# Kernel optimization log

Hardware: AMD Instinct MI355X
Metric: run time of the kernel (lower is better)

The kernel has to match this reference:

```python
import jax, jax.numpy as jnp
import numpy as np

HEADS = 16
EMBD = 1024
D_K = EMBD // HEADS


def setup_inputs() -> dict:
    key = jax.random.key(0)
    ks = jax.random.split(key, 9)
    s = 1.0 / np.sqrt(EMBD)
    inp = {
        "x": jax.random.normal(ks[0], (4, 2048, EMBD), dtype=jnp.float32),
        "w_q": jax.random.normal(ks[1], (EMBD, EMBD), dtype=jnp.float32) * s,
        "b_q": jax.random.normal(ks[2], (EMBD,), dtype=jnp.float32) * 0.01,
        "w_k": jax.random.normal(ks[3], (EMBD, EMBD), dtype=jnp.float32) * s,
        "b_k": jax.random.normal(ks[4], (EMBD,), dtype=jnp.float32) * 0.01,
        "w_v": jax.random.normal(ks[5], (EMBD, EMBD), dtype=jnp.float32) * s,
        "b_v": jax.random.normal(ks[6], (EMBD,), dtype=jnp.float32) * 0.01,
        "w_o": jax.random.normal(ks[7], (EMBD, EMBD), dtype=jnp.float32) * s,
        "b_o": jax.random.normal(ks[8], (EMBD,), dtype=jnp.float32) * 0.01,
    }
    return inp


def reference(x, w_q, b_q, w_k, b_k, w_v, b_v, w_o, b_o):
    b, s, e = x.shape
    # Linear layers (torch Linear: x @ W^T + b; weights stored as [out,in] -> here [in,out] already? We store [in,out])
    q = x @ w_q + b_q
    k = x @ w_k + b_k
    v = x @ w_v + b_v
    # reshape to [b, h, s, d_k]
    qh = q.reshape(b, s, HEADS, D_K).transpose(0, 2, 1, 3)
    kh = k.reshape(b, s, HEADS, D_K).transpose(0, 2, 1, 3)
    vh = v.reshape(b, s, HEADS, D_K).transpose(0, 2, 1, 3)
    scores = jnp.einsum('bhqd,bhkd->bhqk', qh, kh) / jnp.sqrt(jnp.asarray(D_K, x.dtype))
    attn = jax.nn.softmax(scores, axis=-1)
    out = jnp.einsum('bhqk,bhkd->bhqd', attn, vh)
    merged = out.transpose(0, 2, 1, 3).reshape(b, s, e)
    return merged @ w_o + b_o
```

## Files before the change

kernel.cpp:

```cpp
#include <hip/hip_runtime.h>
#include <math.h>

#define B 4
#define S 2048
#define E 1024
#define H 16
#define DK 64
#define NROW (B * S)
#define NT (S / 64)

typedef _Float16 half_t;
typedef __attribute__((ext_vector_type(8))) _Float16 half8;
typedef __attribute__((ext_vector_type(4))) _Float16 half4;
typedef __attribute__((ext_vector_type(4))) float f32x4;

__device__ __forceinline__ void gload_lds16(const void* g, void* l) {
    __builtin_amdgcn_global_load_lds((__attribute__((address_space(1))) void*)(g),
                                     (__attribute__((address_space(3))) void*)(l), 16, 0, 0);
}

__device__ __forceinline__ float fast_exp2(float x) {
    return __builtin_amdgcn_exp2f(x);
}

__global__ __launch_bounds__(256)
void cast_x_kernel(const float* __restrict__ x, half_t* __restrict__ xh) {
    const size_t i = ((size_t)blockIdx.x * 256 + threadIdx.x) * 8;
    float4 a = *(const float4*)(x + i);
    float4 b = *(const float4*)(x + i + 4);
    half8 hv;
    hv[0] = (half_t)a.x; hv[1] = (half_t)a.y; hv[2] = (half_t)a.z; hv[3] = (half_t)a.w;
    hv[4] = (half_t)b.x; hv[5] = (half_t)b.y; hv[6] = (half_t)b.z; hv[7] = (half_t)b.w;
    *(half8*)(xh + i) = hv;
}

__global__ __launch_bounds__(256)
void cast_wT_kernel(const float* __restrict__ w0, const float* __restrict__ w1,
                    const float* __restrict__ w2, const float* __restrict__ w3,
                    half_t* __restrict__ o0, half_t* __restrict__ o1,
                    half_t* __restrict__ o2, half_t* __restrict__ o3) {
    __shared__ half_t Ts[64][72];
    const int z = blockIdx.z;
    const float* W = (z == 0) ? w0 : (z == 1) ? w1 : (z == 2) ? w2 : w3;
    half_t*      O = (z == 0) ? o0 : (z == 1) ? o1 : (z == 2) ? o2 : o3;
    const int t  = threadIdx.x;
    const int k0 = blockIdx.y * 64;
    const int n0 = blockIdx.x * 64;
    const int r  = t >> 2;
    const int c0 = (t & 3) * 16;
    const float* p = W + (size_t)(k0 + r) * E + n0 + c0;
    #pragma unroll
    for (int j = 0; j < 16; j += 4) {
        float4 v = *(const float4*)(p + j);
        Ts[c0 + j + 0][r] = (half_t)v.x;
        Ts[c0 + j + 1][r] = (half_t)v.y;
        Ts[c0 + j + 2][r] = (half_t)v.z;
        Ts[c0 + j + 3][r] = (half_t)v.w;
    }
    __syncthreads();
    half_t* q = O + (size_t)(n0 + r) * E + k0 + c0;
    *(uint4*)(q)     = *(const uint4*)&Ts[r][c0];
    *(uint4*)(q + 8) = *(const uint4*)&Ts[r][c0 + 8];
}

__global__ __launch_bounds__(256)
void gemm_qkv_kernel(const half_t* __restrict__ A, const half_t* __restrict__ Bt,
                     const float* __restrict__ b_q, const float* __restrict__ b_k,
                     const float* __restrict__ b_v,
                     half_t* __restrict__ Qh, half_t* __restrict__ Kh,
                     half_t* __restrict__ Vt) {
    __shared__ half_t SM[128 * 136];
    const int t    = threadIdx.x;
    const int w    = t >> 6;
    const int lane = t & 63;
    const int ln   = t & 15;
    const int qd   = (t >> 4) & 3;
    const int orig = blockIdx.y * 24 + blockIdx.x;
    const int swz  = (orig & 7) * 192 + (orig >> 3);
    const int bn0  = (swz % 24) * 128;
    const int bm0  = (swz / 24) * 128;
    const int wm   = (w & 1) * 64;
    const int wn   = (w >> 1) * 64;
    const int srow = lane >> 2;
    const int sch  = (((lane & 3) ^ (srow & 3)) * 8);
    const int rch  = ((qd ^ (ln & 3)) * 8);

    f32x4 acc[4][4];
    #pragma unroll
    for (int mi = 0; mi < 4; ++mi)
        #pragma unroll
        for (int ni = 0; ni < 4; ++ni) acc[mi][ni] = (f32x4){0.f, 0.f, 0.f, 0.f};

    for (int k0 = 0; k0 < E; k0 += 64) {
        #pragma unroll
        for (int kh = 0; kh < 2; ++kh)
            #pragma unroll
            for (int c = 0; c < 2; ++c) {
                const int rr = c * 64 + w * 16;
                gload_lds16(A  + (size_t)(bm0 + rr + srow) * E + k0 + kh * 32 + sch,
                            SM + kh * 4096 + rr * 32);
                gload_lds16(Bt + (size_t)(bn0 + rr + srow) * E + k0 + kh * 32 + sch,
                            SM + 8192 + kh * 4096 + rr * 32);
            }
        __syncthreads();
        #pragma unroll
        for (int kh = 0; kh < 2; ++kh) {
            half8 af[4], bf[4];
            #pragma unroll
            for (int mi = 0; mi < 4; ++mi)
                af[mi] = *(const half8*)&SM[kh * 4096 + (wm + mi * 16 + ln) * 32 + rch];
            #pragma unroll
            for (int ni = 0; ni < 4; ++ni)
                bf[ni] = *(const half8*)&SM[8192 + kh * 4096 + (wn + ni * 16 + ln) * 32 + rch];
            #pragma unroll
            for (int mi = 0; mi < 4; ++mi)
                #pragma unroll
                for (int ni = 0; ni < 4; ++ni)
                    acc[mi][ni] = __builtin_amdgcn_mfma_f32_16x16x32_f16(af[mi], bf[ni], acc[mi][ni], 0, 0, 0);
        }
        __syncthreads();
    }

    const int route = bn0 >> 10;
    const int nloc0 = bn0 & 1023;
    const float* bp = (route == 0) ? b_q : (route == 1) ? b_k : b_v;
    float bv[4];
    #pragma unroll
    for (int ni = 0; ni < 4; ++ni) bv[ni] = bp[nloc0 + wn + ni * 16 + ln];

    if (route < 2) {
        half_t* Cst = (route == 0) ? Qh : Kh;
        #pragma unroll
        for (int mi = 0; mi < 4; ++mi)
            #pragma unroll
            for (int r = 0; r < 4; ++r) {
                const size_t row = (size_t)(bm0 + wm + mi * 16 + qd * 4 + r);
                #pragma unroll
                for (int ni = 0; ni < 4; ++ni)
                    Cst[row * E + nloc0 + wn + ni * 16 + ln] = (half_t)(acc[mi][ni][r] + bv[ni]);
            }
    } else {
        #pragma unroll
        for (int mi = 0; mi < 4; ++mi)
            #pragma unroll
            for (int ni = 0; ni < 4; ++ni)
                #pragma unroll
                for (int r = 0; r < 4; ++r)
                    SM[(wn + ni * 16 + ln) * 136 + wm + mi * 16 + qd * 4 + r] =
                        (half_t)(acc[mi][ni][r] + bv[ni]);
        __syncthreads();
        const int nl = t >> 1;
        const int sc = (t & 1) * 64;
        const int gv = nloc0 + nl;
        const int hh = gv >> 6, dd = gv & 63;
        const int bb = bm0 >> 11;
        const int sb = (bm0 & (S - 1)) + sc;
        half_t* dst = Vt + ((size_t)(bb * H + hh) * DK + dd) * S + sb;
        const half_t* src = SM + nl * 136 + sc;
        #pragma unroll
        for (int j = 0; j < 64; j += 8)
            *(half8*)(dst + j) = *(const half8*)(src + j);
    }
}

__global__ __launch_bounds__(256)
void gemm_oproj_kernel(const half_t* __restrict__ A, const half_t* __restrict__ Bt,
                       const float* __restrict__ bias, float* __restrict__ Cout) {
    __shared__ half_t SM[2 * 8192];
    const int t    = threadIdx.x;
    const int w    = t >> 6;
    const int lane = t & 63;
    const int ln   = t & 15;
    const int qd   = (t >> 4) & 3;
    const int orig = blockIdx.y * 8 + blockIdx.x;
    const int swz  = (orig & 7) * 64 + (orig >> 3);
    const int bn0  = (swz & 7) * 128;
    const int bm0  = (swz >> 3) * 128;
    const int wm   = (w & 1) * 64;
    const int wn   = (w >> 1) * 64;
    const int srow = lane >> 2;
    const int sch  = (((lane & 3) ^ (srow & 3)) * 8);
    const int rch  = ((qd ^ (ln & 3)) * 8);

    f32x4 acc[4][4];
    #pragma unroll
    for (int mi = 0; mi < 4; ++mi)
        #pragma unroll
        for (int ni = 0; ni < 4; ++ni) acc[mi][ni] = (f32x4){0.f, 0.f, 0.f, 0.f};

    for (int k0 = 0; k0 < E; k0 += 64) {
        #pragma unroll
        for (int kh = 0; kh < 2; ++kh)
            #pragma unroll
            for (int c = 0; c < 2; ++c) {
                const int rr = c * 64 + w * 16;
                gload_lds16(A  + (size_t)(bm0 + rr + srow) * E + k0 + kh * 32 + sch,
                            SM + kh * 4096 + rr * 32);
                gload_lds16(Bt + (size_t)(bn0 + rr + srow) * E + k0 + kh * 32 + sch,
                            SM + 8192 + kh * 4096 + rr * 32);
            }
        __syncthreads();
        #pragma unroll
        for (int kh = 0; kh < 2; ++kh) {
            half8 af[4], bf[4];
            #pragma unroll
            for (int mi = 0; mi < 4; ++mi)
                af[mi] = *(const half8*)&SM[kh * 4096 + (wm + mi * 16 + ln) * 32 + rch];
            #pragma unroll
            for (int ni = 0; ni < 4; ++ni)
                bf[ni] = *(const half8*)&SM[8192 + kh * 4096 + (wn + ni * 16 + ln) * 32 + rch];
            #pragma unroll
            for (int mi = 0; mi < 4; ++mi)
                #pragma unroll
                for (int ni = 0; ni < 4; ++ni)
                    acc[mi][ni] = __builtin_amdgcn_mfma_f32_16x16x32_f16(af[mi], bf[ni], acc[mi][ni], 0, 0, 0);
        }
        __syncthreads();
    }

    float bv[4];
    #pragma unroll
    for (int ni = 0; ni < 4; ++ni) bv[ni] = bias[bn0 + wn + ni * 16 + ln];
    #pragma unroll
    for (int mi = 0; mi < 4; ++mi)
        #pragma unroll
        for (int r = 0; r < 4; ++r) {
            const size_t row = (size_t)(bm0 + wm + mi * 16 + qd * 4 + r);
            #pragma unroll
            for (int ni = 0; ni < 4; ++ni)
                Cout[row * E + bn0 + wn + ni * 16 + ln] = acc[mi][ni][r] + bv[ni];
        }
}

__global__ __launch_bounds__(256, 4)
void attn_kernel7(const half_t* __restrict__ Qg, const half_t* __restrict__ Kg,
                  const half_t* __restrict__ Vtg, half_t* __restrict__ CTX) {
    __shared__ half_t Kbuf[2][4096];
    __shared__ half_t Vbuf[2][4096];

    const int t    = threadIdx.x;
    const int w    = t >> 6;
    const int lane = t & 63;
    const int ln   = t & 15;
    const int qd   = (t >> 4) & 3;
    const int orig = blockIdx.y * 16 + blockIdx.x;
    const int swz  = (orig & 7) * 128 + (orig >> 3);
    const int bh   = swz >> 4;
    const int s0   = (swz & 15) * 128;
    const int b    = bh >> 4;
    const int h    = bh & 15;
    const int q0   = w * 32;

    half8 aq[2][2];
    #pragma unroll
    for (int mt = 0; mt < 2; ++mt)
        #pragma unroll
        for (int kd = 0; kd < 2; ++kd)
            aq[mt][kd] = *(const half8*)(Qg +
                (size_t)(b * S + s0 + q0 + mt * 16 + ln) * E + h * DK + kd * 32 + qd * 8);

    const half_t* kgp = Kg + (size_t)(b * S + w * 16 + ln) * E + h * DK + qd * 8;
    const half_t* vgp = Vtg + (size_t)(bh * DK + w * 16 + (lane & 7)) * S + (lane >> 3) * 8;

    gload_lds16(kgp,      &Kbuf[0][(w * 2 + 0) * 512]);
    gload_lds16(kgp + 32, &Kbuf[0][(w * 2 + 1) * 512]);
    gload_lds16(vgp,                 &Vbuf[0][(w * 2 + 0) * 512]);
    gload_lds16(vgp + (size_t)8 * S, &Vbuf[0][(w * 2 + 1) * 512]);

    f32x4 oacc[2][4];
    #pragma unroll
    for (int mt = 0; mt < 2; ++mt)
        #pragma unroll
        for (int dt = 0; dt < 4; ++dt) oacc[mt][dt] = (f32x4){0.f, 0.f, 0.f, 0.f};
    f32x4 lfrag[2];
    lfrag[0] = (f32x4){0.f, 0.f, 0.f, 0.f};
    lfrag[1] = (f32x4){0.f, 0.f, 0.f, 0.f};

    half8 vone;
    #pragma unroll
    for (int j = 0; j < 8; ++j) vone[j] = (half_t)1;

    const float kexp  = 0.1803368731f;
    const float kbias = 7.2134752f;

    const int vrb = (ln >> 3) * 512 + (ln & 7) * 8 + (qd & 1) * 4 + (qd >> 1) * 64;

    for (int kt = 0; kt < NT; ++kt) {
        const int cur = kt & 1;
        __syncthreads();

        if (kt + 1 < NT) {
            const half_t* kp = kgp + (size_t)(kt + 1) * 64 * E;
            const half_t* vp = vgp + (kt + 1) * 64;
            gload_lds16(kp,      &Kbuf[1 - cur][(w * 2 + 0) * 512]);
            gload_lds16(kp + 32, &Kbuf[1 - cur][(w * 2 + 1) * 512]);
            gload_lds16(vp,                 &Vbuf[1 - cur][(w * 2 + 0) * 512]);
            gload_lds16(vp + (size_t)8 * S, &Vbuf[1 - cur][(w * 2 + 1) * 512]);
        }

        half8 kf[4][2];
        #pragma unroll
        for (int ct = 0; ct < 4; ++ct)
            #pragma unroll
            for (int kd = 0; kd < 2; ++kd)
                kf[ct][kd] = *(const half8*)&Kbuf[cur][(ct * 2 + kd) * 512 + lane * 8];

        half8 vf[4][2];
        const half_t* vb = &Vbuf[cur][vrb];
        #pragma unroll
        for (int dt = 0; dt < 4; ++dt)
            #pragma unroll
            for (int kq = 0; kq < 2; ++kq) {
                union { half4 h4[2]; half8 h8; } u;
                u.h4[0] = *(const half4*)(vb + dt * 1024 + kq * 256);
                u.h4[1] = *(const half4*)(vb + dt * 1024 + kq * 256 + 128);
                vf[dt][kq] = u.h8;
            }

        #pragma unroll
        for (int mt = 0; mt < 2; ++mt) {
            f32x4 sacc[4];
            #pragma unroll
            for (int ct = 0; ct < 4; ++ct) {
                f32x4 sv = (f32x4){0.f, 0.f, 0.f, 0.f};
                sv = __builtin_amdgcn_mfma_f32_16x16x32_f16(kf[ct][0], aq[mt][0], sv, 0, 0, 0);
                sv = __builtin_amdgcn_mfma_f32_16x16x32_f16(kf[ct][1], aq[mt][1], sv, 0, 0, 0);
                sacc[ct] = sv;
            }
            half8 pa[2];
            #pragma unroll
            for (int kq = 0; kq < 2; ++kq)
                #pragma unroll
                for (int j = 0; j < 8; ++j) {
                    const int ct = kq * 2 + (j >> 2);
                    const int r  = j & 3;
                    pa[kq][j] = (half_t)fast_exp2(fmaf(sacc[ct][r], kexp, -kbias));
                }

            lfrag[mt] = __builtin_amdgcn_mfma_f32_16x16x32_f16(pa[0], vone, lfrag[mt], 0, 0, 0);
            lfrag[mt] = __builtin_amdgcn_mfma_f32_16x16x32_f16(pa[1], vone, lfrag[mt], 0, 0, 0);
            #pragma unroll
            for (int dt = 0; dt < 4; ++dt) {
                oacc[mt][dt] = __builtin_amdgcn_mfma_f32_16x16x32_f16(pa[0], vf[dt][0], oacc[mt][dt], 0, 0, 0);
                oacc[mt][dt] = __builtin_amdgcn_mfma_f32_16x16x32_f16(pa[1], vf[dt][1], oacc[mt][dt], 0, 0, 0);
            }
        }
    }

    #pragma unroll
    for (int mt = 0; mt < 2; ++mt)
        #pragma unroll
        for (int r = 0; r < 4; ++r) {
            const float invl = 1.f / lfrag[mt][r];
            const size_t row = (size_t)(b * S + s0 + q0 + mt * 16 + qd * 4 + r);
            #pragma unroll
            for (int dt = 0; dt < 4; ++dt)
                CTX[row * E + h * DK + dt * 16 + ln] = (half_t)(oacc[mt][dt][r] * invl);
        }
}

extern "C" void kernel_launch(void* const* d_in, const int* in_sizes, int n_in,
                              void* d_out, int out_size, void* d_ws, size_t ws_size,
                              hipStream_t stream) {
    const float* x   = (const float*)d_in[0];
    const float* w_q = (const float*)d_in[1];
    const float* b_q = (const float*)d_in[2];
    const float* w_k = (const float*)d_in[3];
    const float* b_k = (const float*)d_in[4];
    const float* w_v = (const float*)d_in[5];
    const float* b_v = (const float*)d_in[6];
    const float* w_o = (const float*)d_in[7];
    const float* b_o = (const float*)d_in[8];
    float* out = (float*)d_out;

    half_t* xh  = (half_t*)d_ws;
    half_t* Wt3 = xh  + (size_t)NROW * E;
    half_t* WtO = Wt3 + (size_t)3 * E * E;
    half_t* Qh  = WtO + (size_t)E * E;
    half_t* Kh  = Qh  + (size_t)NROW * E;
    half_t* Vt  = Kh  + (size_t)NROW * E;
    half_t* CTX = Vt  + (size_t)NROW * E;

    cast_x_kernel<<<dim3(NROW * E / (256 * 8)), dim3(256), 0, stream>>>(x, xh);
    cast_wT_kernel<<<dim3(16, 16, 4), dim3(256), 0, stream>>>(
        w_q, w_k, w_v, w_o,
        Wt3, Wt3 + (size_t)E * E, Wt3 + (size_t)2 * E * E, WtO);

    gemm_qkv_kernel<<<dim3(3 * E / 128, NROW / 128), dim3(256), 0, stream>>>(
        xh, Wt3, b_q, b_k, b_v, Qh, Kh, Vt);

    attn_kernel7<<<dim3(S / 128, B * H), dim3(256), 0, stream>>>(Qh, Kh, Vt, CTX);

    gemm_oproj_kernel<<<dim3(E / 128, NROW / 128), dim3(256), 0, stream>>>(CTX, WtO, b_o, out);
}
```

Baseline: 284.5 us.

## Triple-buffer K/V tiles in attention with two-ahead prefetch and vmcnt waits

The attention kernel now uses three LDS buffers for K and V instead of two and prefetches tiles two iterations ahead. __syncthreads is replaced by an explicit s_waitcnt vmcnt(4) plus s_barrier, so only the older tile's loads must finish before compute starts. This hides more global-load latency, but LDS use per block rises by half and launch bounds drop from 4 to 3 blocks per CU, which lowers occupancy.

```diff
diff --git a/kernel.cpp b/kernel.cpp
--- a/kernel.cpp
+++ b/kernel.cpp
@@ -232,11 +232,11 @@
         }
 }
 
-__global__ __launch_bounds__(256, 4)
-void attn_kernel7(const half_t* __restrict__ Qg, const half_t* __restrict__ Kg,
+__global__ __launch_bounds__(256, 3)
+void attn_kernel8(const half_t* __restrict__ Qg, const half_t* __restrict__ Kg,
                   const half_t* __restrict__ Vtg, half_t* __restrict__ CTX) {
-    __shared__ half_t Kbuf[2][4096];
-    __shared__ half_t Vbuf[2][4096];
+    __shared__ half_t Kbuf[3][4096];
+    __shared__ half_t Vbuf[3][4096];
 
     const int t    = threadIdx.x;
     const int w    = t >> 6;
@@ -262,10 +262,15 @@
     const half_t* kgp = Kg + (size_t)(b * S + w * 16 + ln) * E + h * DK + qd * 8;
     const half_t* vgp = Vtg + (size_t)(bh * DK + w * 16 + (lane & 7)) * S + (lane >> 3) * 8;
 
-    gload_lds16(kgp,      &Kbuf[0][(w * 2 + 0) * 512]);
-    gload_lds16(kgp + 32, &Kbuf[0][(w * 2 + 1) * 512]);
-    gload_lds16(vgp,                 &Vbuf[0][(w * 2 + 0) * 512]);
-    gload_lds16(vgp + (size_t)8 * S, &Vbuf[0][(w * 2 + 1) * 512]);
+    #pragma unroll
+    for (int p = 0; p < 2; ++p) {
+        const half_t* kp = kgp + (size_t)p * 64 * E;
+        const half_t* vp = vgp + p * 64;
+        gload_lds16(kp,      &Kbuf[p][(w * 2 + 0) * 512]);
+        gload_lds16(kp + 32, &Kbuf[p][(w * 2 + 1) * 512]);
+        gload_lds16(vp,                 &Vbuf[p][(w * 2 + 0) * 512]);
+        gload_lds16(vp + (size_t)8 * S, &Vbuf[p][(w * 2 + 1) * 512]);
+    }
 
     f32x4 oacc[2][4];
     #pragma unroll
@@ -286,17 +291,21 @@
     const int vrb = (ln >> 3) * 512 + (ln & 7) * 8 + (qd & 1) * 4 + (qd >> 1) * 64;
 
     for (int kt = 0; kt < NT; ++kt) {
-        const int cur = kt & 1;
-        __syncthreads();
-
-        if (kt + 1 < NT) {
-            const half_t* kp = kgp + (size_t)(kt + 1) * 64 * E;
-            const half_t* vp = vgp + (kt + 1) * 64;
-            gload_lds16(kp,      &Kbuf[1 - cur][(w * 2 + 0) * 512]);
-            gload_lds16(kp + 32, &Kbuf[1 - cur][(w * 2 + 1) * 512]);
-            gload_lds16(vp,                 &Vbuf[1 - cur][(w * 2 + 0) * 512]);
-            gload_lds16(vp + (size_t)8 * S, &Vbuf[1 - cur][(w * 2 + 1) * 512]);
-        }
+        if (kt < NT - 1) asm volatile("s_waitcnt vmcnt(4)" ::: "memory");
+        else             asm volatile("s_waitcnt vmcnt(0)" ::: "memory");
+        __builtin_amdgcn_s_barrier();
+
+        if (kt + 2 < NT) {
+            const int sb = (kt + 2) % 3;
+            const half_t* kp = kgp + (size_t)(kt + 2) * 64 * E;
+            const half_t* vp = vgp + (kt + 2) * 64;
+            gload_lds16(kp,      &Kbuf[sb][(w * 2 + 0) * 512]);
+            gload_lds16(kp + 32, &Kbuf[sb][(w * 2 + 1) * 512]);
+            gload_lds16(vp,                 &Vbuf[sb][(w * 2 + 0) * 512]);
+            gload_lds16(vp + (size_t)8 * S, &Vbuf[sb][(w * 2 + 1) * 512]);
+        }
+
+        const int cur = kt % 3;
 
         half8 kf[4][2];
         #pragma unroll
@@ -389,7 +398,7 @@
     gemm_qkv_kernel<<<dim3(3 * E / 128, NROW / 128), dim3(256), 0, stream>>>(
         xh, Wt3, b_q, b_k, b_v, Qh, Kh, Vt);
 
-    attn_kernel7<<<dim3(S / 128, B * H), dim3(256), 0, stream>>>(Qh, Kh, Vt, CTX);
+    attn_kernel8<<<dim3(S / 128, B * H), dim3(256), 0, stream>>>(Qh, Kh, Vt, CTX);
 
     gemm_oproj_kernel<<<dim3(E / 128, NROW / 128), dim3(256), 0, stream>>>(CTX, WtO, b_o, out);
 }
```

Measured after the change: 302.3 us. 6.2% more time.
